# Optimization experiments

Measured on AMD Instinct MI355X. Metric: run time of the kernel, lower is better.

The kernel has to match this reference:

```python
import jax, jax.numpy as jnp
import numpy as np

N_WIRES = 8
DIM = 2 ** N_WIRES  # 256 amplitudes
# PauliZ sign table: Z_SIGNS[w, i] = +1 if bit w of basis index i is 0 else -1
_bits = (np.arange(DIM)[None, :] >> (N_WIRES - 1 - np.arange(N_WIRES))[:, None]) & 1
Z_SIGNS = jnp.asarray(1.0 - 2.0 * _bits, dtype=jnp.float32)  # [8, 256]


def quantum_project(t, theta):
    """Batched 8-wire circuit: RX(x_w) encoder + trainable RX(theta_w) (RX gates on the
    same wire compose additively), then CNOT ring, then <Z_w> for each wire.
    t: [B, S, E] -> returns [B, S, H, 8]."""
    B, S, E = t.shape
    H = E // N_WIRES
    ang = (t.reshape(B, S, H, N_WIRES) + theta) * 0.5  # RX(a)RX(b)=RX(a+b)
    q0 = jnp.cos(ang).astype(jnp.complex64)
    q1 = (-1j * jnp.sin(ang)).astype(jnp.complex64)
    # Build product state |psi> = \otimes_w [cos(a_w/2), -i sin(a_w/2)] -> [B,S,H,256]
    state = jnp.ones((B, S, H, 1), jnp.complex64)
    for w in range(N_WIRES):
        qb = jnp.stack([q0[..., w], q1[..., w]], axis=-1)  # [B,S,H,2]
        state = (state[..., :, None] * qb[..., None, :]).reshape(B, S, H, -1)
    state = state.reshape((B, S, H) + (2,) * N_WIRES)  # wire w on axis 3+w
    # CNOT chain 0->1,...,6->7 then ring-closing 7->0
    for cw, tw in [(w, w + 1) for w in range(N_WIRES - 1)] + [(N_WIRES - 1, 0)]:
        s0 = jax.lax.index_in_dim(state, 0, axis=3 + cw, keepdims=True)
        s1 = jnp.flip(jax.lax.index_in_dim(state, 1, axis=3 + cw, keepdims=True), axis=3 + tw)
        state = jnp.concatenate([s0, s1], axis=3 + cw)
    amps = state.reshape(B, S, H, DIM)
    probs = amps.real * amps.real + amps.imag * amps.imag  # [B,S,H,256] float32
    return jnp.einsum('bshd,wd->bshw', probs, Z_SIGNS)  # <Z_w> per wire


def setup_inputs() -> dict:
    key = jax.random.key(0)
    kx, kq, kk, kv, ko, kt = jax.random.split(key, 6)
    B, S, E = 16, 512, 64
    scale = 1.0 / np.sqrt(E)
    return {
        'x': jax.random.normal(kx, (B, S, E), dtype=jnp.float32),
        'Wq': jax.random.normal(kq, (E, E), dtype=jnp.float32) * scale,
        'Wk': jax.random.normal(kk, (E, E), dtype=jnp.float32) * scale,
        'Wv': jax.random.normal(kv, (E, E), dtype=jnp.float32) * scale,
        'Wo': jax.random.normal(ko, (E, E), dtype=jnp.float32) * scale,
        'theta': jax.random.uniform(kt, (N_WIRES,), dtype=jnp.float32, minval=0.0, maxval=2.0 * np.pi),
    }


def reference(x, Wq, Wk, Wv, Wo, theta):
    B, S, E = x.shape
    q = quantum_project(x @ Wq.T, theta)  # [B,S,H,8]
    k = quantum_project(x @ Wk.T, theta)
    v = quantum_project(x @ Wv.T, theta)
    # NOTE: original code never transposes heads to dim 1, so attention mixes HEADS
    # per token: scores [B,S,H,H]. Faithfully reproduced. d_k = 8.
    scores = jnp.einsum('bsiw,bsjw->bsij', q, k) / jnp.float32(np.sqrt(N_WIRES))
    attn = jax.nn.softmax(scores, axis=-1)  # dropout is identity in eval
    out = jnp.einsum('bsij,bsjw->bsiw', attn, v)  # [B,S,H,8]
    # original: out.transpose(1,2).contiguous().view(B,-1,E) -> scrambled layout
    out = out.transpose(0, 2, 1, 3).reshape(B, -1, E)
    return out @ Wo.T
```

## Files before the change

### kernel.cpp

```cpp
#include <hip/hip_runtime.h>


#define WT  4096
#define SPS 68
#define SCS 68

#define DPP_SHR_STEP(d, j, sh)                                                 \
    {                                                                          \
        float _t = __int_as_float(__builtin_amdgcn_update_dpp(                 \
            0x3f800000, __float_as_int(d), 0x110 + sh, 0xf, 0xf, false));      \
        d *= ((j) >= (sh)) ? _t : 1.0f;                                        \
    }

__device__ __forceinline__ float rl(float v, int l) {
    return __int_as_float(__builtin_amdgcn_readlane(__float_as_int(v), l));
}

__global__ __launch_bounds__(256, 2)
void qattn_fused(const float* __restrict__ xg,
                 const float* __restrict__ wqg, const float* __restrict__ wkg,
                 const float* __restrict__ wvg, const float* __restrict__ wog,
                 const float* __restrict__ thg,
                 float* __restrict__ outg)
{
    __shared__ float sWt[3 * WT];
    __shared__ __align__(16) float sP[48 * SPS];
    __shared__ __align__(16) float sScr[16 * SCS];

    const int tid  = threadIdx.x;
    const int lane = tid & 63;
    const int wg   = tid >> 6;
    const int j    = lane & 7;
    const int b    = blockIdx.x >> 5;
    const int grp  = blockIdx.x & 31;

    {
        const float* gm[3] = {wqg, wkg, wvg};
        #pragma unroll
        for (int m = 0; m < 3; ++m) {
            #pragma unroll
            for (int r = 0; r < 4; ++r) {
                const int g = tid + 256 * r;
                const float4 v = ((const float4*)gm[m])[g];
                const int e = g >> 4, kq = g & 15;
                const int c0 = (2 * e + 4 * kq) & 127;
                const int c1 = (c0 + 2) & 127;
                *(float2*)&sWt[m * WT + 256 * kq + c0]       = make_float2(v.x, v.y);
                *(float2*)&sWt[m * WT + 256 * kq + 128 + c1] = make_float2(v.z, v.w);
            }
        }
    }
    float xr[4];
    {
        const float* xb = xg + ((size_t)(b * 512 + grp * 16 + wg * 4)) * 64 + lane;
        xr[0] = xb[0]; xr[1] = xb[64]; xr[2] = xb[128]; xr[3] = xb[192];
    }
    const float thf = thg[j];
    __syncthreads();

    {
        float acc[3][4];
        #pragma unroll
        for (int m = 0; m < 3; ++m)
            #pragma unroll
            for (int t = 0; t < 4; ++t) acc[m][t] = 0.f;

        #pragma unroll 8
        for (int kk = 0; kk < 32; ++kk) {
            const int col = (2 * lane + 2 * kk) & 127;
            const float2 wq = *(const float2*)&sWt[0 * WT + kk * 128 + col];
            const float2 wk = *(const float2*)&sWt[1 * WT + kk * 128 + col];
            const float2 wv = *(const float2*)&sWt[2 * WT + kk * 128 + col];
            #pragma unroll
            for (int t = 0; t < 4; ++t) {
                const float x0 = rl(xr[t], 2 * kk);
                const float x1 = rl(xr[t], 2 * kk + 1);
                acc[0][t] = fmaf(wq.x, x0, fmaf(wq.y, x1, acc[0][t]));
                acc[1][t] = fmaf(wk.x, x0, fmaf(wk.y, x1, acc[1][t]));
                acc[2][t] = fmaf(wv.x, x0, fmaf(wv.y, x1, acc[2][t]));
            }
        }
        #pragma unroll
        for (int m = 0; m < 3; ++m) {
            #pragma unroll
            for (int t = 0; t < 4; ++t) {
                const float c = __cosf(acc[m][t] + thf);
                float d = c;
                DPP_SHR_STEP(d, j, 1)
                DPP_SHR_STEP(d, j, 2)
                DPP_SHR_STEP(d, j, 4)
                float ex = (j == 0) ? 1.0f : c;
                DPP_SHR_STEP(ex, j, 1)
                DPP_SHR_STEP(ex, j, 2)
                DPP_SHR_STEP(ex, j, 4)
                const int base = ((wg * 3 + m) * 4 + t) * SPS + lane;
                if (j > 0)  sP[base]     = d;
                if (j == 7) sP[base - 7] = ex;
            }
        }
    }

    {
        const int t  = lane >> 4;
        const int i  = j;
        const int tt = wg * 4 + t;
        const int qb = ((wg * 3 + 0) * 4 + t) * SPS;
        const int kb = ((wg * 3 + 1) * 4 + t) * SPS;
        const int vb = ((wg * 3 + 2) * 4 + t) * SPS;
        float q[8];
        *(float4*)&q[0] = *(const float4*)&sP[qb + 8 * i];
        *(float4*)&q[4] = *(const float4*)&sP[qb + 8 * i + 4];
        float p[8];
        float sum = 0.f;
        #pragma unroll
        for (int jj = 0; jj < 8; ++jj) {
            const float4 k0 = *(const float4*)&sP[kb + 8 * jj];
            const float4 k1 = *(const float4*)&sP[kb + 8 * jj + 4];
            float s = q[0] * k0.x;
            s = fmaf(q[1], k0.y, s); s = fmaf(q[2], k0.z, s);
            s = fmaf(q[3], k0.w, s); s = fmaf(q[4], k1.x, s);
            s = fmaf(q[5], k1.y, s); s = fmaf(q[6], k1.z, s);
            s = fmaf(q[7], k1.w, s);
            p[jj] = __expf(s * 0.35355339059327373f);
            sum += p[jj];
        }
        const float rinv = 1.0f / sum;
        float o[8];
        #pragma unroll
        for (int w = 0; w < 8; ++w) o[w] = 0.f;
        #pragma unroll
        for (int jj = 0; jj < 8; ++jj) {
            const float4 v0 = *(const float4*)&sP[vb + 8 * jj];
            const float4 v1 = *(const float4*)&sP[vb + 8 * jj + 4];
            const float a = p[jj] * rinv;
            o[0] = fmaf(a, v0.x, o[0]); o[1] = fmaf(a, v0.y, o[1]);
            o[2] = fmaf(a, v0.z, o[2]); o[3] = fmaf(a, v0.w, o[3]);
            o[4] = fmaf(a, v1.x, o[4]); o[5] = fmaf(a, v1.y, o[5]);
            o[6] = fmaf(a, v1.z, o[6]); o[7] = fmaf(a, v1.w, o[7]);
        }
        if (!(lane & 8)) {
            float* sd = &sScr[(i * 2 + (tt >> 3)) * SCS + 8 * (tt & 7)];
            *(float4*)sd       = make_float4(o[0], o[1], o[2], o[3]);
            *(float4*)(sd + 4) = make_float4(o[4], o[5], o[6], o[7]);
        }
    }
    __syncthreads();

    {
        float wo[64];
        #pragma unroll
        for (int kc = 0; kc < 16; ++kc) {
            const float4 v = *(const float4*)(wog + lane * 64 + kc * 4);
            wo[4 * kc] = v.x; wo[4 * kc + 1] = v.y;
            wo[4 * kc + 2] = v.z; wo[4 * kc + 3] = v.w;
        }
        #pragma unroll
        for (int rr = 0; rr < 4; ++rr) {
            const int rho = wg * 4 + rr;
            const float sv = sScr[rho * SCS + lane];
            float y0 = 0.f, y1 = 0.f, y2 = 0.f, y3 = 0.f;
            #pragma unroll
            for (int k = 0; k < 64; k += 4) {
                y0 = fmaf(wo[k],     rl(sv, k),     y0);
                y1 = fmaf(wo[k + 1], rl(sv, k + 1), y1);
                y2 = fmaf(wo[k + 2], rl(sv, k + 2), y2);
                y3 = fmaf(wo[k + 3], rl(sv, k + 3), y3);
            }
            const float y = (y0 + y1) + (y2 + y3);
            const int head = rho >> 1, oct = rho & 1;
            outg[((size_t)(b * 512 + head * 64 + grp * 2 + oct)) * 64 + lane] = y;
        }
    }
}

extern "C" void kernel_launch(void* const* d_in, const int* in_sizes, int n_in,
                              void* d_out, int out_size, void* d_ws, size_t ws_size,
                              hipStream_t stream) {
    const float* x  = (const float*)d_in[0];
    const float* wq = (const float*)d_in[1];
    const float* wk = (const float*)d_in[2];
    const float* wv = (const float*)d_in[3];
    const float* wo = (const float*)d_in[4];
    const float* th = (const float*)d_in[5];
    float* out = (float*)d_out;
    qattn_fused<<<dim3(512), dim3(256), 0, stream>>>(x, wq, wk, wv, wo, th, out);
}
```

Measured before the change: 75.28 us.

## Split K-reduction across two wave halves with 512-thread blocks and staged Wo

Doubles the block to 512 threads. Each half of the waves computes half of the K-reduction for the QKV projection, and the partial sums are combined through shared memory before the cosine/product-state step. Idle waves stage Wo into shared memory (reusing the QKV weight buffer), so the output projection reads Wo from LDS instead of each lane loading its row from global memory. This adds two extra barriers and more waves per block, and depends on reaching 4 blocks per CU at about 70KB of LDS per block.

```diff
diff --git a/kernel.cpp b/kernel.cpp
--- a/kernel.cpp
+++ b/kernel.cpp
@@ -4,6 +4,7 @@
 #define WT  4096
 #define SPS 68
 #define SCS 68
+#define WOS 66
 
 #define DPP_SHR_STEP(d, j, sh)                                                 \
     {                                                                          \
@@ -16,7 +17,7 @@
     return __int_as_float(__builtin_amdgcn_readlane(__float_as_int(v), l));
 }
 
-__global__ __launch_bounds__(256, 2)
+__global__ __launch_bounds__(512, 4)
 void qattn_fused(const float* __restrict__ xg,
                  const float* __restrict__ wqg, const float* __restrict__ wkg,
                  const float* __restrict__ wvg, const float* __restrict__ wog,
@@ -26,10 +27,13 @@
     __shared__ float sWt[3 * WT];
     __shared__ __align__(16) float sP[48 * SPS];
     __shared__ __align__(16) float sScr[16 * SCS];
+    float* sWo = sWt;
 
     const int tid  = threadIdx.x;
     const int lane = tid & 63;
     const int wg   = tid >> 6;
+    const int p    = wg & 3;
+    const int half = wg >> 2;
     const int j    = lane & 7;
     const int b    = blockIdx.x >> 5;
     const int grp  = blockIdx.x & 31;
@@ -39,8 +43,8 @@
         #pragma unroll
         for (int m = 0; m < 3; ++m) {
             #pragma unroll
-            for (int r = 0; r < 4; ++r) {
-                const int g = tid + 256 * r;
+            for (int r = 0; r < 2; ++r) {
+                const int g = tid + 512 * r;
                 const float4 v = ((const float4*)gm[m])[g];
                 const int e = g >> 4, kq = g & 15;
                 const int c0 = (2 * e + 4 * kq) & 127;
@@ -52,39 +56,53 @@
     }
     float xr[4];
     {
-        const float* xb = xg + ((size_t)(b * 512 + grp * 16 + wg * 4)) * 64 + lane;
+        const float* xb = xg + ((size_t)(b * 512 + grp * 16 + p * 4)) * 64 + lane;
         xr[0] = xb[0]; xr[1] = xb[64]; xr[2] = xb[128]; xr[3] = xb[192];
     }
     const float thf = thg[j];
     __syncthreads();
 
-    {
-        float acc[3][4];
-        #pragma unroll
-        for (int m = 0; m < 3; ++m)
-            #pragma unroll
-            for (int t = 0; t < 4; ++t) acc[m][t] = 0.f;
-
+    float acc[3][4];
+    #pragma unroll
+    for (int m = 0; m < 3; ++m)
+        #pragma unroll
+        for (int t = 0; t < 4; ++t) acc[m][t] = 0.f;
+    {
+        const int kb0 = half * 16;
         #pragma unroll 8
-        for (int kk = 0; kk < 32; ++kk) {
-            const int col = (2 * lane + 2 * kk) & 127;
-            const float2 wq = *(const float2*)&sWt[0 * WT + kk * 128 + col];
-            const float2 wk = *(const float2*)&sWt[1 * WT + kk * 128 + col];
-            const float2 wv = *(const float2*)&sWt[2 * WT + kk * 128 + col];
+        for (int kk = 0; kk < 16; ++kk) {
+            const int kkg = kb0 + kk;
+            const int col = (2 * lane + 2 * kkg) & 127;
+            const float2 wq = *(const float2*)&sWt[0 * WT + kkg * 128 + col];
+            const float2 wk = *(const float2*)&sWt[1 * WT + kkg * 128 + col];
+            const float2 wv = *(const float2*)&sWt[2 * WT + kkg * 128 + col];
             #pragma unroll
             for (int t = 0; t < 4; ++t) {
-                const float x0 = rl(xr[t], 2 * kk);
-                const float x1 = rl(xr[t], 2 * kk + 1);
+                const float x0 = rl(xr[t], 2 * kkg);
+                const float x1 = rl(xr[t], 2 * kkg + 1);
                 acc[0][t] = fmaf(wq.x, x0, fmaf(wq.y, x1, acc[0][t]));
                 acc[1][t] = fmaf(wk.x, x0, fmaf(wk.y, x1, acc[1][t]));
                 acc[2][t] = fmaf(wv.x, x0, fmaf(wv.y, x1, acc[2][t]));
             }
         }
+    }
+    if (half == 0) {
+        #pragma unroll
+        for (int m = 0; m < 3; ++m)
+            #pragma unroll
+            for (int t = 0; t < 4; ++t)
+                sP[((p * 3 + m) * 4 + t) * SPS + lane] = acc[m][t];
+    }
+    __syncthreads();
+
+    if (half == 1) {
         #pragma unroll
         for (int m = 0; m < 3; ++m) {
             #pragma unroll
             for (int t = 0; t < 4; ++t) {
-                const float c = __cosf(acc[m][t] + thf);
+                const int base = ((p * 3 + m) * 4 + t) * SPS + lane;
+                const float ang = acc[m][t] + sP[base] + thf;
+                const float c = __cosf(ang);
                 float d = c;
                 DPP_SHR_STEP(d, j, 1)
                 DPP_SHR_STEP(d, j, 2)
@@ -93,24 +111,35 @@
                 DPP_SHR_STEP(ex, j, 1)
                 DPP_SHR_STEP(ex, j, 2)
                 DPP_SHR_STEP(ex, j, 4)
-                const int base = ((wg * 3 + m) * 4 + t) * SPS + lane;
                 if (j > 0)  sP[base]     = d;
                 if (j == 7) sP[base - 7] = ex;
             }
         }
-    }
-
-    {
-        const int t  = lane >> 4;
+    } else if (wg >= 2) {
+        const int lt = tid - 128;
+        #pragma unroll
+        for (int r = 0; r < 8; ++r) {
+            const int g = lt + 128 * r;
+            const float4 v = ((const float4*)wog)[g];
+            const int e = g >> 4, kq = g & 15;
+            float* d = &sWo[e * WOS + 4 * kq];
+            *(float2*)d       = make_float2(v.x, v.y);
+            *(float2*)(d + 2) = make_float2(v.z, v.w);
+        }
+    }
+    __syncthreads();
+
+    if (wg < 2) {
+        const int tg = wg * 8 + (lane >> 3);
         const int i  = j;
-        const int tt = wg * 4 + t;
-        const int qb = ((wg * 3 + 0) * 4 + t) * SPS;
-        const int kb = ((wg * 3 + 1) * 4 + t) * SPS;
-        const int vb = ((wg * 3 + 2) * 4 + t) * SPS;
+        const int p2 = tg >> 2, t2 = tg & 3;
+        const int qb = ((p2 * 3 + 0) * 4 + t2) * SPS;
+        const int kb = ((p2 * 3 + 1) * 4 + t2) * SPS;
+        const int vb = ((p2 * 3 + 2) * 4 + t2) * SPS;
         float q[8];
         *(float4*)&q[0] = *(const float4*)&sP[qb + 8 * i];
         *(float4*)&q[4] = *(const float4*)&sP[qb + 8 * i + 4];
-        float p[8];
+        float pr[8];
         float sum = 0.f;
         #pragma unroll
         for (int jj = 0; jj < 8; ++jj) {
@@ -121,8 +150,8 @@
             s = fmaf(q[3], k0.w, s); s = fmaf(q[4], k1.x, s);
             s = fmaf(q[5], k1.y, s); s = fmaf(q[6], k1.z, s);
             s = fmaf(q[7], k1.w, s);
-            p[jj] = __expf(s * 0.35355339059327373f);
-            sum += p[jj];
+            pr[jj] = __expf(s * 0.35355339059327373f);
+            sum += pr[jj];
         }
         const float rinv = 1.0f / sum;
         float o[8];
@@ -132,31 +161,28 @@
         for (int jj = 0; jj < 8; ++jj) {
             const float4 v0 = *(const float4*)&sP[vb + 8 * jj];
             const float4 v1 = *(const float4*)&sP[vb + 8 * jj + 4];
-            const float a = p[jj] * rinv;
+            const float a = pr[jj] * rinv;
             o[0] = fmaf(a, v0.x, o[0]); o[1] = fmaf(a, v0.y, o[1]);
             o[2] = fmaf(a, v0.z, o[2]); o[3] = fmaf(a, v0.w, o[3]);
             o[4] = fmaf(a, v1.x, o[4]); o[5] = fmaf(a, v1.y, o[5]);
             o[6] = fmaf(a, v1.z, o[6]); o[7] = fmaf(a, v1.w, o[7]);
         }
-        if (!(lane & 8)) {
-            float* sd = &sScr[(i * 2 + (tt >> 3)) * SCS + 8 * (tt & 7)];
-            *(float4*)sd       = make_float4(o[0], o[1], o[2], o[3]);
-            *(float4*)(sd + 4) = make_float4(o[4], o[5], o[6], o[7]);
-        }
+        float* sd = &sScr[(i * 2 + (tg >> 3)) * SCS + 8 * (tg & 7)];
+        *(float4*)sd       = make_float4(o[0], o[1], o[2], o[3]);
+        *(float4*)(sd + 4) = make_float4(o[4], o[5], o[6], o[7]);
     }
     __syncthreads();
 
     {
         float wo[64];
         #pragma unroll
-        for (int kc = 0; kc < 16; ++kc) {
-            const float4 v = *(const float4*)(wog + lane * 64 + kc * 4);
-            wo[4 * kc] = v.x; wo[4 * kc + 1] = v.y;
-            wo[4 * kc + 2] = v.z; wo[4 * kc + 3] = v.w;
-        }
-        #pragma unroll
-        for (int rr = 0; rr < 4; ++rr) {
-            const int rho = wg * 4 + rr;
+        for (int c = 0; c < 32; ++c) {
+            const float2 v = *(const float2*)&sWo[lane * WOS + 2 * c];
+            wo[2 * c] = v.x; wo[2 * c + 1] = v.y;
+        }
+        #pragma unroll
+        for (int rr = 0; rr < 2; ++rr) {
+            const int rho = wg * 2 + rr;
             const float sv = sScr[rho * SCS + lane];
             float y0 = 0.f, y1 = 0.f, y2 = 0.f, y3 = 0.f;
             #pragma unroll
@@ -183,5 +209,5 @@
     const float* wo = (const float*)d_in[4];
     const float* th = (const float*)d_in[5];
     float* out = (float*)d_out;
-    qattn_fused<<<dim3(512), dim3(256), 0, stream>>>(x, wq, wk, wv, wo, th, out);
+    qattn_fused<<<dim3(512), dim3(512), 0, stream>>>(x, wq, wk, wv, wo, th, out);
 }
```

After: 73.28 us. 1.03x faster.

## Use split-bf16 MFMA for QKV and output projections with larger blocks

Applied to the files above, without the earlier changes.

Replaces the scalar FMA/readlane projections for Q/K/V and the Wo output projection with 16x16x32 bf16 MFMA instructions. Each fp32 value is split into high and low bf16 parts and three MFMAs are accumulated to approximate fp32 accuracy. Blocks now handle 32 tokens with 512 threads (256 blocks), and Wo is staged into shared memory alongside the other weights. This trades extra conversion work, more LDS and fewer, larger blocks for matrix-core throughput in place of VALU and readlane costs.

```diff
diff --git a/kernel.cpp b/kernel.cpp
--- a/kernel.cpp
+++ b/kernel.cpp
@@ -1,9 +1,13 @@
 #include <hip/hip_runtime.h>
 
 
-#define WT  4096
+typedef float  f32x4  __attribute__((ext_vector_type(4)));
+typedef short  bf16x8 __attribute__((ext_vector_type(8)));
+typedef unsigned short u16;
+typedef unsigned int   u32;
+
+#define WRS 72
 #define SPS 68
-#define SCS 68
 
 #define DPP_SHR_STEP(d, j, sh)                                                 \
     {                                                                          \
@@ -12,105 +16,119 @@
         d *= ((j) >= (sh)) ? _t : 1.0f;                                        \
     }
 
-__device__ __forceinline__ float rl(float v, int l) {
-    return __int_as_float(__builtin_amdgcn_readlane(__float_as_int(v), l));
-}
-
-__global__ __launch_bounds__(256, 2)
+__device__ __forceinline__ u32 bfh(float f) {
+    const u32 u = __float_as_uint(f);
+    return (u + 0x7FFFu + ((u >> 16) & 1u)) >> 16;
+}
+__device__ __forceinline__ void bfsplit(float f, u32& h, u32& l) {
+    h = bfh(f);
+    l = bfh(f - __uint_as_float(h << 16));
+}
+
+#define MFMA3(acc, ah, al, bh, bl)                                             \
+    acc = __builtin_amdgcn_mfma_f32_16x16x32_bf16(al, bh, acc, 0, 0, 0);       \
+    acc = __builtin_amdgcn_mfma_f32_16x16x32_bf16(ah, bl, acc, 0, 0, 0);       \
+    acc = __builtin_amdgcn_mfma_f32_16x16x32_bf16(ah, bh, acc, 0, 0, 0);
+
+__global__ __launch_bounds__(512, 1)
 void qattn_fused(const float* __restrict__ xg,
                  const float* __restrict__ wqg, const float* __restrict__ wkg,
                  const float* __restrict__ wvg, const float* __restrict__ wog,
                  const float* __restrict__ thg,
                  float* __restrict__ outg)
 {
-    __shared__ float sWt[3 * WT];
-    __shared__ __align__(16) float sP[48 * SPS];
-    __shared__ __align__(16) float sScr[16 * SCS];
+    __shared__ u16 sWh[4 * 64 * WRS];
+    __shared__ u16 sWl[4 * 64 * WRS];
+    __shared__ u16 sXh[32 * WRS];
+    __shared__ u16 sXl[32 * WRS];
+    __shared__ __align__(16) float sP[96 * SPS];
+    __shared__ u16 sSh[32 * WRS];
+    __shared__ u16 sSl[32 * WRS];
 
     const int tid  = threadIdx.x;
     const int lane = tid & 63;
     const int wg   = tid >> 6;
+    const int l15  = lane & 15;
+    const int quad = lane >> 4;
     const int j    = lane & 7;
-    const int b    = blockIdx.x >> 5;
-    const int grp  = blockIdx.x & 31;
+    const int b    = blockIdx.x >> 4;
+    const int grp  = blockIdx.x & 15;
 
     {
-        const float* gm[3] = {wqg, wkg, wvg};
-        #pragma unroll
-        for (int m = 0; m < 3; ++m) {
-            #pragma unroll
-            for (int r = 0; r < 4; ++r) {
-                const int g = tid + 256 * r;
-                const float4 v = ((const float4*)gm[m])[g];
-                const int e = g >> 4, kq = g & 15;
-                const int c0 = (2 * e + 4 * kq) & 127;
-                const int c1 = (c0 + 2) & 127;
-                *(float2*)&sWt[m * WT + 256 * kq + c0]       = make_float2(v.x, v.y);
-                *(float2*)&sWt[m * WT + 256 * kq + 128 + c1] = make_float2(v.z, v.w);
-            }
-        }
-    }
-    float xr[4];
+        const float* gm[4] = {wqg, wkg, wvg, wog};
+        #pragma unroll
+        for (int r = 0; r < 8; ++r) {
+            const int m   = r >> 1;
+            const int idx = (r & 1) * 512 + tid;
+            const float4 v = ((const float4*)gm[m])[idx];
+            const int e = idx >> 4, c = idx & 15;
+            u32 h0, l0, h1, l1, h2, l2, h3, l3;
+            bfsplit(v.x, h0, l0); bfsplit(v.y, h1, l1);
+            bfsplit(v.z, h2, l2); bfsplit(v.w, h3, l3);
+            const int o = (m * 64 + e) * WRS + 4 * c;
+            *(uint2*)&sWh[o] = make_uint2(h0 | (h1 << 16), h2 | (h3 << 16));
+            *(uint2*)&sWl[o] = make_uint2(l0 | (l1 << 16), l2 | (l3 << 16));
+        }
+    }
     {
-        const float* xb = xg + ((size_t)(b * 512 + grp * 16 + wg * 4)) * 64 + lane;
-        xr[0] = xb[0]; xr[1] = xb[64]; xr[2] = xb[128]; xr[3] = xb[192];
+        const float4 v = ((const float4*)(xg + (size_t)(b * 512 + grp * 32) * 64))[tid];
+        const int t = tid >> 4, c = tid & 15;
+        u32 h0, l0, h1, l1, h2, l2, h3, l3;
+        bfsplit(v.x, h0, l0); bfsplit(v.y, h1, l1);
+        bfsplit(v.z, h2, l2); bfsplit(v.w, h3, l3);
+        const int o = t * WRS + 4 * c;
+        *(uint2*)&sXh[o] = make_uint2(h0 | (h1 << 16), h2 | (h3 << 16));
+        *(uint2*)&sXl[o] = make_uint2(l0 | (l1 << 16), l2 | (l3 << 16));
     }
     const float thf = thg[j];
     __syncthreads();
 
-    {
-        float acc[3][4];
-        #pragma unroll
-        for (int m = 0; m < 3; ++m)
-            #pragma unroll
-            for (int t = 0; t < 4; ++t) acc[m][t] = 0.f;
-
-        #pragma unroll 8
-        for (int kk = 0; kk < 32; ++kk) {
-            const int col = (2 * lane + 2 * kk) & 127;
-            const float2 wq = *(const float2*)&sWt[0 * WT + kk * 128 + col];
-            const float2 wk = *(const float2*)&sWt[1 * WT + kk * 128 + col];
-            const float2 wv = *(const float2*)&sWt[2 * WT + kk * 128 + col];
-            #pragma unroll
-            for (int t = 0; t < 4; ++t) {
-                const float x0 = rl(xr[t], 2 * kk);
-                const float x1 = rl(xr[t], 2 * kk + 1);
-                acc[0][t] = fmaf(wq.x, x0, fmaf(wq.y, x1, acc[0][t]));
-                acc[1][t] = fmaf(wk.x, x0, fmaf(wk.y, x1, acc[1][t]));
-                acc[2][t] = fmaf(wv.x, x0, fmaf(wv.y, x1, acc[2][t]));
-            }
-        }
-        #pragma unroll
-        for (int m = 0; m < 3; ++m) {
-            #pragma unroll
-            for (int t = 0; t < 4; ++t) {
-                const float c = __cosf(acc[m][t] + thf);
-                float d = c;
-                DPP_SHR_STEP(d, j, 1)
-                DPP_SHR_STEP(d, j, 2)
-                DPP_SHR_STEP(d, j, 4)
-                float ex = (j == 0) ? 1.0f : c;
-                DPP_SHR_STEP(ex, j, 1)
-                DPP_SHR_STEP(ex, j, 2)
-                DPP_SHR_STEP(ex, j, 4)
-                const int base = ((wg * 3 + m) * 4 + t) * SPS + lane;
-                if (j > 0)  sP[base]     = d;
-                if (j == 7) sP[base - 7] = ex;
-            }
-        }
-    }
-
-    {
-        const int t  = lane >> 4;
+    #pragma unroll
+    for (int ia = 0; ia < 3; ++ia) {
+        const int aid = wg * 3 + ia;
+        const int mt = aid & 1, nt = (aid >> 1) & 3, m = aid >> 3;
+        const int arow = (mt * 16 + l15) * WRS + quad * 8;
+        const int brow = (m * 64 + nt * 16 + l15) * WRS + quad * 8;
+        const bf16x8 ah0 = *(const bf16x8*)&sXh[arow];
+        const bf16x8 ah1 = *(const bf16x8*)&sXh[arow + 32];
+        const bf16x8 al0 = *(const bf16x8*)&sXl[arow];
+        const bf16x8 al1 = *(const bf16x8*)&sXl[arow + 32];
+        const bf16x8 bh0 = *(const bf16x8*)&sWh[brow];
+        const bf16x8 bh1 = *(const bf16x8*)&sWh[brow + 32];
+        const bf16x8 bl0 = *(const bf16x8*)&sWl[brow];
+        const bf16x8 bl1 = *(const bf16x8*)&sWl[brow + 32];
+        f32x4 acc = {0.f, 0.f, 0.f, 0.f};
+        MFMA3(acc, ah0, al0, bh0, bl0)
+        MFMA3(acc, ah1, al1, bh1, bl1)
+        #pragma unroll
+        for (int r = 0; r < 4; ++r) {
+            const float c = __cosf(acc[r] + thf);
+            float d = c;
+            DPP_SHR_STEP(d, j, 1)
+            DPP_SHR_STEP(d, j, 2)
+            DPP_SHR_STEP(d, j, 4)
+            float ex = (j == 0) ? 1.0f : c;
+            DPP_SHR_STEP(ex, j, 1)
+            DPP_SHR_STEP(ex, j, 2)
+            DPP_SHR_STEP(ex, j, 4)
+            const int row  = m * 32 + mt * 16 + quad * 4 + r;
+            const int base = row * SPS + nt * 16 + l15;
+            if (j > 0)  sP[base]     = d;
+            if (j == 7) sP[base - 7] = ex;
+        }
+    }
+    __syncthreads();
+
+    if (wg < 4) {
+        const int tg = wg * 8 + (lane >> 3);
         const int i  = j;
-        const int tt = wg * 4 + t;
-        const int qb = ((wg * 3 + 0) * 4 + t) * SPS;
-        const int kb = ((wg * 3 + 1) * 4 + t) * SPS;
-        const int vb = ((wg * 3 + 2) * 4 + t) * SPS;
+        const int qb = tg * SPS;
+        const int kb = (32 + tg) * SPS;
+        const int vb = (64 + tg) * SPS;
         float q[8];
         *(float4*)&q[0] = *(const float4*)&sP[qb + 8 * i];
         *(float4*)&q[4] = *(const float4*)&sP[qb + 8 * i + 4];
-        float p[8];
+        float pr[8];
         float sum = 0.f;
         #pragma unroll
         for (int jj = 0; jj < 8; ++jj) {
@@ -121,8 +139,8 @@
             s = fmaf(q[3], k0.w, s); s = fmaf(q[4], k1.x, s);
             s = fmaf(q[5], k1.y, s); s = fmaf(q[6], k1.z, s);
             s = fmaf(q[7], k1.w, s);
-            p[jj] = __expf(s * 0.35355339059327373f);
-            sum += p[jj];
+            pr[jj] = __expf(s * 0.35355339059327373f);
+            sum += pr[jj];
         }
         const float rinv = 1.0f / sum;
         float o[8];
@@ -132,43 +150,48 @@
         for (int jj = 0; jj < 8; ++jj) {
             const float4 v0 = *(const float4*)&sP[vb + 8 * jj];
             const float4 v1 = *(const float4*)&sP[vb + 8 * jj + 4];
-            const float a = p[jj] * rinv;
+            const float a = pr[jj] * rinv;
             o[0] = fmaf(a, v0.x, o[0]); o[1] = fmaf(a, v0.y, o[1]);
             o[2] = fmaf(a, v0.z, o[2]); o[3] = fmaf(a, v0.w, o[3]);
             o[4] = fmaf(a, v1.x, o[4]); o[5] = fmaf(a, v1.y, o[5]);
             o[6] = fmaf(a, v1.z, o[6]); o[7] = fmaf(a, v1.w, o[7]);
         }
-        if (!(lane & 8)) {
-            float* sd = &sScr[(i * 2 + (tt >> 3)) * SCS + 8 * (tt & 7)];
-            *(float4*)sd       = make_float4(o[0], o[1], o[2], o[3]);
-            *(float4*)(sd + 4) = make_float4(o[4], o[5], o[6], o[7]);
-        }
+        u32 hh[4], ll[4];
+        #pragma unroll
+        for (int c = 0; c < 4; ++c) {
+            u32 ha, la, hb, lb;
+            bfsplit(o[2 * c], ha, la);
+            bfsplit(o[2 * c + 1], hb, lb);
+            hh[c] = ha | (hb << 16);
+            ll[c] = la | (lb << 16);
+        }
+        const int so = (i * 4 + (tg >> 3)) * WRS + 8 * (tg & 7);
+        *(uint4*)&sSh[so] = make_uint4(hh[0], hh[1], hh[2], hh[3]);
+        *(uint4*)&sSl[so] = make_uint4(ll[0], ll[1], ll[2], ll[3]);
     }
     __syncthreads();
 
     {
-        float wo[64];
-        #pragma unroll
-        for (int kc = 0; kc < 16; ++kc) {
-            const float4 v = *(const float4*)(wog + lane * 64 + kc * 4);
-            wo[4 * kc] = v.x; wo[4 * kc + 1] = v.y;
-            wo[4 * kc + 2] = v.z; wo[4 * kc + 3] = v.w;
-        }
-        #pragma unroll
-        for (int rr = 0; rr < 4; ++rr) {
-            const int rho = wg * 4 + rr;
-            const float sv = sScr[rho * SCS + lane];
-            float y0 = 0.f, y1 = 0.f, y2 = 0.f, y3 = 0.f;
-            #pragma unroll
-            for (int k = 0; k < 64; k += 4) {
-                y0 = fmaf(wo[k],     rl(sv, k),     y0);
-                y1 = fmaf(wo[k + 1], rl(sv, k + 1), y1);
-                y2 = fmaf(wo[k + 2], rl(sv, k + 2), y2);
-                y3 = fmaf(wo[k + 3], rl(sv, k + 3), y3);
-            }
-            const float y = (y0 + y1) + (y2 + y3);
-            const int head = rho >> 1, oct = rho & 1;
-            outg[((size_t)(b * 512 + head * 64 + grp * 2 + oct)) * 64 + lane] = y;
+        const int mt2 = wg >> 2, nt2 = wg & 3;
+        const int arow = (mt2 * 16 + l15) * WRS + quad * 8;
+        const int brow = (3 * 64 + nt2 * 16 + l15) * WRS + quad * 8;
+        const bf16x8 ah0 = *(const bf16x8*)&sSh[arow];
+        const bf16x8 ah1 = *(const bf16x8*)&sSh[arow + 32];
+        const bf16x8 al0 = *(const bf16x8*)&sSl[arow];
+        const bf16x8 al1 = *(const bf16x8*)&sSl[arow + 32];
+        const bf16x8 bh0 = *(const bf16x8*)&sWh[brow];
+        const bf16x8 bh1 = *(const bf16x8*)&sWh[brow + 32];
+        const bf16x8 bl0 = *(const bf16x8*)&sWl[brow];
+        const bf16x8 bl1 = *(const bf16x8*)&sWl[brow + 32];
+        f32x4 acc = {0.f, 0.f, 0.f, 0.f};
+        MFMA3(acc, ah0, al0, bh0, bl0)
+        MFMA3(acc, ah1, al1, bh1, bl1)
+        const int e = nt2 * 16 + l15;
+        #pragma unroll
+        for (int r = 0; r < 4; ++r) {
+            const int rho = mt2 * 16 + quad * 4 + r;
+            const int R   = (rho >> 2) * 64 + grp * 4 + (rho & 3);
+            outg[((size_t)(b * 512 + R)) * 64 + e] = acc[r];
         }
     }
 }
@@ -183,5 +206,5 @@
     const float* wo = (const float*)d_in[4];
     const float* th = (const float*)d_in[5];
     float* out = (float*)d_out;
-    qattn_fused<<<dim3(512), dim3(256), 0, stream>>>(x, wq, wk, wv, wo, th, out);
-}
+    qattn_fused<<<dim3(256), dim3(512), 0, stream>>>(x, wq, wk, wv, wo, th, out);
+}
```

After: 67.59 us (median of 2 runs). 10.2% less time.
